# Kernel optimization log

Hardware: AMD Instinct MI355X
Metric: run time of the kernel (lower is better)

The kernel has to match this reference:

```python
import jax, jax.numpy as jnp
import numpy as np

B, N, CQ, H, CH = 1, 256, 128, 4, 32  # batch, n_res, c_q(=c_k=c_v), heads, per-head dim


def setup_inputs() -> dict:
    key = jax.random.key(0)
    ks = jax.random.split(key, 12)
    s = 0.02
    q_x = jax.random.normal(ks[0], (B, N, N, CQ), jnp.float32)
    kv_x = jax.random.normal(ks[1], (B, N, N, CQ), jnp.float32)
    # mask bias: 0 where kept, -1e9 where masked (additive mask)
    keep = jax.random.uniform(ks[2], (B, N, 1, 1, N)) < 0.9
    mask_bias = jnp.where(keep, 0.0, -1e9).astype(jnp.float32)
    triangle_bias = jax.random.normal(ks[3], (B, 1, H, N, N), jnp.float32)
    # projection weights, stored per-head as [H, CH, C_in]
    wq = jax.random.normal(ks[4], (H, CH, CQ), jnp.float32) * s
    wk = jax.random.normal(ks[5], (H, CH, CQ), jnp.float32) * s
    wv = jax.random.normal(ks[6], (H, CH, CQ), jnp.float32) * s
    wg = jax.random.normal(ks[7], (H, CH, CQ), jnp.float32) * s
    bg = jax.random.normal(ks[8], (H, CH), jnp.float32) * s + 1.0  # gating bias init 1
    wo = jax.random.normal(ks[9], (CQ, H * CH), jnp.float32) * s
    bo = jnp.zeros((CQ,), jnp.float32)
    return {"q_x": q_x, "kv_x": kv_x, "mask_bias": mask_bias,
            "triangle_bias": triangle_bias, "wq": wq, "wk": wk, "wv": wv,
            "wg": wg, "bg": bg, "wo": wo, "bo": bo}


def reference(q_x, kv_x, mask_bias, triangle_bias, wq, wk, wv, wg, bg, wo, bo):
    scale = 1.0 / np.sqrt(CH).astype(np.float32)
    # project + split heads: [B,N,Q,C] x [H,D,C] -> [B,N,H,Q,D]
    q = jnp.einsum('bnqc,hdc->bnhqd', q_x, wq) * scale
    k = jnp.einsum('bnkc,hdc->bnhkd', kv_x, wk)
    v = jnp.einsum('bnkc,hdc->bnhkd', kv_x, wv)
    # scores + additive biases (mask_bias broadcasts over h,q; triangle over n)
    a = jnp.einsum('bnhqd,bnhkd->bnhqk', q, k) + mask_bias + triangle_bias
    a = jax.nn.softmax(a, axis=-1)
    o = jnp.einsum('bnhqk,bnhkd->bnhqd', a, v)
    o = jnp.swapaxes(o, -2, -3)  # [B,N,Q,H,D]
    # gating
    g = jax.nn.sigmoid(jnp.einsum('bnqc,hdc->bnqhd', q_x, wg) + bg)
    o = o * g
    o = o.reshape(o.shape[:-2] + (H * CH,))  # [B,N,Q,H*D]
    return jnp.einsum('bnqe,ce->bnqc', o, wo) + bo
```

## Files before the change

### kernel.cpp

```cpp
#include <hip/hip_runtime.h>

#define NRES 256
#define CIN  128
#define NH   4
#define DH   32

#define KST 32
#define VST 264
#define PST 40
#define GST 136

typedef __attribute__((ext_vector_type(4))) float f32x4;
typedef __attribute__((ext_vector_type(8))) short bf16x8;

__device__ __forceinline__ unsigned pkbf(float a, float b) {
    unsigned ua = __builtin_bit_cast(unsigned, a);
    unsigned ub = __builtin_bit_cast(unsigned, b);
    ua += 0x7fffu + ((ua >> 16) & 1u);
    ub += 0x7fffu + ((ub >> 16) & 1u);
    return __builtin_amdgcn_perm(ub, ua, 0x07060302);
}
__device__ __forceinline__ unsigned short f2bfu(float f) {
    unsigned u = __builtin_bit_cast(unsigned, f);
    return (unsigned short)((u + 0x7fffu + ((u >> 16) & 1u)) >> 16);
}
union bfr { unsigned u[4]; bf16x8 v; };
__device__ __forceinline__ bf16x8 ldcvt8(const float* __restrict__ p) {
    f32x4 a = *(const f32x4*)p; f32x4 b = *(const f32x4*)(p + 4);
    bfr r;
    r.u[0] = pkbf(a[0], a[1]); r.u[1] = pkbf(a[2], a[3]);
    r.u[2] = pkbf(b[0], b[1]); r.u[3] = pkbf(b[2], b[3]);
    return r.v;
}
__device__ __forceinline__ bf16x8 ldcvt8s(const float* __restrict__ p, float sc) {
    f32x4 a = *(const f32x4*)p; f32x4 b = *(const f32x4*)(p + 4);
    bfr r;
    r.u[0] = pkbf(a[0] * sc, a[1] * sc); r.u[1] = pkbf(a[2] * sc, a[3] * sc);
    r.u[2] = pkbf(b[0] * sc, b[1] * sc); r.u[3] = pkbf(b[2] * sc, b[3] * sc);
    return r.v;
}
#define MFMA(a, b, c) __builtin_amdgcn_mfma_f32_16x16x32_bf16((a), (b), (c), 0, 0, 0)

__global__ __launch_bounds__(256, 3) void attn_mfma(
    const float* __restrict__ q_x, const float* __restrict__ kv_x,
    const float* __restrict__ mask_bias, const float* __restrict__ tri_bias,
    const float* __restrict__ wq, const float* __restrict__ wk,
    const float* __restrict__ wv, float* __restrict__ o_out)
{
    const int h = blockIdx.x, n = blockIdx.y;
    const int t = threadIdx.x;
    const int lane = t & 63, w = t >> 6;
    const int mrow = lane & 15;
    const int grp  = lane >> 4;
    const int koff = grp * 8;
    const int rbase = grp * 4;
    const int q0 = w * 64;

    __shared__ unsigned short Ks[NRES * KST];
    __shared__ unsigned short Vt[DH * VST];
    __shared__ unsigned short Pt[4 * 32 * PST];
    __shared__ float msk[NRES];

    if (t < 64) *(float4*)&msk[t * 4] = *(const float4*)(mask_bias + n * NRES + t * 4);

    const float* __restrict__ qxn = q_x  + (size_t)n * NRES * CIN;
    const float* __restrict__ kxn = kv_x + (size_t)n * NRES * CIN;
    const float* __restrict__ wqh = wq + h * DH * CIN;
    const float* __restrict__ wkh = wk + h * DH * CIN;
    const float* __restrict__ wvh = wv + h * DH * CIN;

    f32x4 aq_[4][2], ak_[4][2], av_[4][2];
    const f32x4 zf = {0.f, 0.f, 0.f, 0.f};
    #pragma unroll
    for (int qt = 0; qt < 4; ++qt)
        #pragma unroll
        for (int dt = 0; dt < 2; ++dt) { aq_[qt][dt] = zf; ak_[qt][dt] = zf; av_[qt][dt] = zf; }

    const float qsc = 0.17677669529663687f;
    #pragma unroll
    for (int ct = 0; ct < 4; ++ct) {
        const int c0 = ct * 32 + koff;
        bf16x8 bq0 = ldcvt8s(wqh + mrow * CIN + c0, qsc);
        bf16x8 bq1 = ldcvt8s(wqh + (16 + mrow) * CIN + c0, qsc);
        bf16x8 bk0 = ldcvt8(wkh + mrow * CIN + c0);
        bf16x8 bk1 = ldcvt8(wkh + (16 + mrow) * CIN + c0);
        bf16x8 bv0 = ldcvt8(wvh + mrow * CIN + c0);
        bf16x8 bv1 = ldcvt8(wvh + (16 + mrow) * CIN + c0);
        #pragma unroll
        for (int qt = 0; qt < 4; ++qt) {
            bf16x8 aX = ldcvt8(qxn + (q0 + qt * 16 + mrow) * CIN + c0);
            aq_[qt][0] = MFMA(aX, bq0, aq_[qt][0]);
            aq_[qt][1] = MFMA(aX, bq1, aq_[qt][1]);
            bf16x8 aK = ldcvt8(kxn + (q0 + qt * 16 + mrow) * CIN + c0);
            ak_[qt][0] = MFMA(aK, bk0, ak_[qt][0]);
            ak_[qt][1] = MFMA(aK, bk1, ak_[qt][1]);
            av_[qt][0] = MFMA(aK, bv0, av_[qt][0]);
            av_[qt][1] = MFMA(aK, bv1, av_[qt][1]);
        }
    }

    #pragma unroll
    for (int qt = 0; qt < 4; ++qt)
        #pragma unroll
        for (int dt = 0; dt < 2; ++dt)
            #pragma unroll
            for (int r = 0; r < 4; ++r) {
                const int row = q0 + qt * 16 + rbase + r;
                const int d = dt * 16 + mrow;
                Ks[row * KST + d] = f2bfu(ak_[qt][dt][r]);
                Vt[d * VST + row] = f2bfu(av_[qt][dt][r]);
            }

    unsigned short* __restrict__ pw = &Pt[w * 32 * PST];
    bf16x8 aq[4];
    #pragma unroll
    for (int h2 = 0; h2 < 2; ++h2) {
        #pragma unroll
        for (int j = 0; j < 2; ++j) {
            const int qt = h2 * 2 + j;
            #pragma unroll
            for (int dt = 0; dt < 2; ++dt)
                #pragma unroll
                for (int r = 0; r < 4; ++r)
                    pw[(j * 16 + rbase + r) * PST + dt * 16 + mrow] = f2bfu(aq_[qt][dt][r]);
        }
        asm volatile("s_waitcnt lgkmcnt(0)" ::: "memory");
        #pragma unroll
        for (int j = 0; j < 2; ++j)
            aq[h2 * 2 + j] = *(const bf16x8*)&pw[(j * 16 + mrow) * PST + koff];
        asm volatile("s_waitcnt lgkmcnt(0)" ::: "memory");
    }
    __syncthreads();

    f32x4 oa[4][2], ls4[4];
    #pragma unroll
    for (int qt = 0; qt < 4; ++qt) { oa[qt][0] = zf; oa[qt][1] = zf; ls4[qt] = zf; }

    const float* __restrict__ trih = tri_bias + (size_t)h * NRES * NRES;

    for (int kt = 0; kt < 8; ++kt) {
        const int kb = kt * 32;
        bf16x8 bk0 = *(const bf16x8*)&Ks[(kb + mrow) * KST + koff];
        bf16x8 bk1 = *(const bf16x8*)&Ks[(kb + 16 + mrow) * KST + koff];
        bf16x8 bv0 = *(const bf16x8*)&Vt[mrow * VST + kb + koff];
        bf16x8 bv1 = *(const bf16x8*)&Vt[(16 + mrow) * VST + kb + koff];
        const float mb0 = msk[kb + mrow] - 8.f;
        const float mb1 = msk[kb + 16 + mrow] - 8.f;

        #pragma unroll
        for (int h2 = 0; h2 < 2; ++h2) {
            float tr0[2][4], tr1[2][4];
            #pragma unroll
            for (int j = 0; j < 2; ++j) {
                const int qt = h2 * 2 + j;
                const float* __restrict__ trow =
                    trih + (q0 + qt * 16 + rbase) * NRES + kb + mrow;
                #pragma unroll
                for (int r = 0; r < 4; ++r) {
                    tr0[j][r] = trow[r * NRES];
                    tr1[j][r] = trow[r * NRES + 16];
                }
            }
            #pragma unroll
            for (int j = 0; j < 2; ++j) {
                const int qt = h2 * 2 + j;
                f32x4 s0 = MFMA(aq[qt], bk0, zf);
                f32x4 s1 = MFMA(aq[qt], bk1, zf);
                #pragma unroll
                for (int r = 0; r < 4; ++r) {
                    s0[r] = __expf(s0[r] + tr0[j][r] + mb0);
                    s1[r] = __expf(s1[r] + tr1[j][r] + mb1);
                }
                ls4[qt] += s0 + s1;
                #pragma unroll
                for (int r = 0; r < 4; ++r) {
                    pw[(j * 16 + rbase + r) * PST + mrow]      = f2bfu(s0[r]);
                    pw[(j * 16 + rbase + r) * PST + 16 + mrow] = f2bfu(s1[r]);
                }
            }
            asm volatile("s_waitcnt lgkmcnt(0)" ::: "memory");
            #pragma unroll
            for (int j = 0; j < 2; ++j) {
                const int qt = h2 * 2 + j;
                bf16x8 pa = *(const bf16x8*)&pw[(j * 16 + mrow) * PST + koff];
                oa[qt][0] = MFMA(pa, bv0, oa[qt][0]);
                oa[qt][1] = MFMA(pa, bv1, oa[qt][1]);
            }
        }
    }

    float* __restrict__ orow = o_out + (size_t)n * NRES * CIN + h * DH;
    #pragma unroll
    for (int qt = 0; qt < 4; ++qt) {
        f32x4 lv = ls4[qt];
        #pragma unroll
        for (int xm = 1; xm < 16; xm <<= 1) {
            lv[0] += __shfl_xor(lv[0], xm, 64);
            lv[1] += __shfl_xor(lv[1], xm, 64);
            lv[2] += __shfl_xor(lv[2], xm, 64);
            lv[3] += __shfl_xor(lv[3], xm, 64);
        }
        #pragma unroll
        for (int r = 0; r < 4; ++r) {
            const float inv = 1.f / lv[r];
            const int q = q0 + qt * 16 + rbase + r;
            orow[q * CIN + mrow]      = oa[qt][0][r] * inv;
            orow[q * CIN + 16 + mrow] = oa[qt][1][r] * inv;
        }
    }
}

__global__ __launch_bounds__(256, 4) void gate_out(
    const float* __restrict__ q_x, const float* __restrict__ wg,
    const float* __restrict__ bg, const float* __restrict__ wo,
    const float* __restrict__ bo, float* __restrict__ io)
{
    const int t = threadIdx.x;
    const int lane = t & 63, w = t >> 6;
    const int mrow = lane & 15, grp = lane >> 4;
    const int koff = grp * 8, rbase = grp * 4;
    const int r0 = blockIdx.x * 128 + w * 32;

    __shared__ unsigned short Gt[4 * 32 * GST];
    unsigned short* __restrict__ gw = &Gt[w * 32 * GST];

    const f32x4 zf = {0.f, 0.f, 0.f, 0.f};
    f32x4 acc[2][8];
    #pragma unroll
    for (int at = 0; at < 2; ++at)
        #pragma unroll
        for (int nt = 0; nt < 8; ++nt) acc[at][nt] = zf;

    #pragma unroll
    for (int ks = 0; ks < 4; ++ks) {
        const int c0 = ks * 32 + koff;
        bf16x8 ax0 = ldcvt8(q_x + (size_t)(r0 + mrow) * CIN + c0);
        bf16x8 ax1 = ldcvt8(q_x + (size_t)(r0 + 16 + mrow) * CIN + c0);
        #pragma unroll
        for (int nt = 0; nt < 8; ++nt) {
            bf16x8 bw = ldcvt8(wg + (nt * 16 + mrow) * CIN + c0);
            acc[0][nt] = MFMA(ax0, bw, acc[0][nt]);
            acc[1][nt] = MFMA(ax1, bw, acc[1][nt]);
        }
    }

    #pragma unroll
    for (int nt = 0; nt < 8; ++nt) {
        const float bge = bg[nt * 16 + mrow];
        #pragma unroll
        for (int at = 0; at < 2; ++at)
            #pragma unroll
            for (int r = 0; r < 4; ++r) {
                const int qg = r0 + at * 16 + rbase + r;
                const float ov = io[(size_t)qg * CIN + nt * 16 + mrow];
                const float g = 1.f / (1.f + __expf(-(acc[at][nt][r] + bge)));
                gw[(at * 16 + rbase + r) * GST + nt * 16 + mrow] = f2bfu(ov * g);
            }
    }
    asm volatile("s_waitcnt lgkmcnt(0)" ::: "memory");

    f32x4 acc2[2][8];
    #pragma unroll
    for (int at = 0; at < 2; ++at)
        #pragma unroll
        for (int nt = 0; nt < 8; ++nt) acc2[at][nt] = zf;

    #pragma unroll
    for (int ks = 0; ks < 4; ++ks) {
        const int e0 = ks * 32 + koff;
        bf16x8 ag0 = *(const bf16x8*)&gw[mrow * GST + e0];
        bf16x8 ag1 = *(const bf16x8*)&gw[(16 + mrow) * GST + e0];
        #pragma unroll
        for (int nt = 0; nt < 8; ++nt) {
            bf16x8 bw = ldcvt8(wo + (nt * 16 + mrow) * CIN + e0);
            acc2[0][nt] = MFMA(ag0, bw, acc2[0][nt]);
            acc2[1][nt] = MFMA(ag1, bw, acc2[1][nt]);
        }
    }

    #pragma unroll
    for (int nt = 0; nt < 8; ++nt) {
        const float boc = bo[nt * 16 + mrow];
        #pragma unroll
        for (int at = 0; at < 2; ++at)
            #pragma unroll
            for (int r = 0; r < 4; ++r)
                io[(size_t)(r0 + at * 16 + rbase + r) * CIN + nt * 16 + mrow] =
                    acc2[at][nt][r] + boc;
    }
}

extern "C" void kernel_launch(void* const* d_in, const int* in_sizes, int n_in,
                              void* d_out, int out_size, void* d_ws, size_t ws_size,
                              hipStream_t stream) {
    const float* q_x  = (const float*)d_in[0];
    const float* kv_x = (const float*)d_in[1];
    const float* mask = (const float*)d_in[2];
    const float* tri  = (const float*)d_in[3];
    const float* wq   = (const float*)d_in[4];
    const float* wk   = (const float*)d_in[5];
    const float* wv   = (const float*)d_in[6];
    const float* wg   = (const float*)d_in[7];
    const float* bg   = (const float*)d_in[8];
    const float* wo   = (const float*)d_in[9];
    const float* bo   = (const float*)d_in[10];
    float* out = (float*)d_out;

    attn_mfma<<<dim3(NH, NRES), 256, 0, stream>>>(q_x, kv_x, mask, tri, wq, wk, wv, out);
    gate_out<<<(NRES * NRES) / 128, 256, 0, stream>>>(q_x, wg, bg, wo, bo, out);
}
```

Before: 270.6 us.

## Hoist QKV and gate projections out of per-head attention into workspace kernels

Restructures the pipeline into four kernels. A one-time bf16 conversion of the weights is followed by a batched projection kernel that computes Q, K, V and the sigmoid gate once per row and writes them to workspace as bf16. A flash-style attention kernel then reads them, applies the gate in its epilogue, and a final kernel does the output projection. Previously each head's block recomputed the K/V projections over the full kv row, and the gate GEMM was done separately. The trade is extra global traffic for the bf16 intermediates, a large workspace requirement, and a fallback to the old path when the workspace is too small.

```diff
diff --git a/kernel.cpp b/kernel.cpp
--- a/kernel.cpp
+++ b/kernel.cpp
@@ -5,13 +5,18 @@
 #define NH   4
 #define DH   32
 
-#define KST 32
-#define VST 264
-#define PST 40
-#define GST 136
-
 typedef __attribute__((ext_vector_type(4))) float f32x4;
 typedef __attribute__((ext_vector_type(8))) short bf16x8;
+typedef unsigned short u16;
+
+#define U_WQG 0
+#define U_WKV 32768
+#define U_WWO 65536
+#define U_QB  131072
+#define U_KB  (U_QB + 8388608)
+#define U_VT  (U_KB + 8388608)
+#define U_GB  (U_VT + 8388608)
+#define WS_NEED ((size_t)(U_GB + 8388608) * 2)
 
 __device__ __forceinline__ unsigned pkbf(float a, float b) {
     unsigned ua = __builtin_bit_cast(unsigned, a);
@@ -20,9 +25,13 @@
     ub += 0x7fffu + ((ub >> 16) & 1u);
     return __builtin_amdgcn_perm(ub, ua, 0x07060302);
 }
-__device__ __forceinline__ unsigned short f2bfu(float f) {
+__device__ __forceinline__ u16 f2bfu(float f) {
     unsigned u = __builtin_bit_cast(unsigned, f);
-    return (unsigned short)((u + 0x7fffu + ((u >> 16) & 1u)) >> 16);
+    return (u16)((u + 0x7fffu + ((u >> 16) & 1u)) >> 16);
+}
+__device__ __forceinline__ float bf2f(u16 v) {
+    unsigned u = ((unsigned)v) << 16;
+    return __builtin_bit_cast(float, u);
 }
 union bfr { unsigned u[4]; bf16x8 v; };
 __device__ __forceinline__ bf16x8 ldcvt8(const float* __restrict__ p) {
@@ -41,7 +50,249 @@
 }
 #define MFMA(a, b, c) __builtin_amdgcn_mfma_f32_16x16x32_bf16((a), (b), (c), 0, 0, 0)
 
-__global__ __launch_bounds__(256, 3) void attn_mfma(
+__global__ void wconv(const float* __restrict__ wq, const float* __restrict__ wk,
+                      const float* __restrict__ wv, const float* __restrict__ wg,
+                      const float* __restrict__ wo, u16* __restrict__ ws)
+{
+    const int i0 = (blockIdx.x * 256 + threadIdx.x) * 8;
+    const float qsc = 0.17677669529663687f;
+    const float* src; u16* dst; float sc = 1.f;
+    if (i0 < 32768) {
+        const int e = i0 >> 7, c = i0 & 127;
+        src = (e < 128 ? wq + e * CIN : wg + (e - 128) * CIN) + c;
+        if (e < 128) sc = qsc;
+        dst = ws + U_WQG + i0;
+    } else if (i0 < 65536) {
+        const int j = i0 - 32768, e = j >> 7, c = j & 127;
+        src = (e < 128 ? wk + e * CIN : wv + (e - 128) * CIN) + c;
+        dst = ws + U_WKV + j;
+    } else {
+        const int j = i0 - 65536;
+        src = wo + j; dst = ws + U_WWO + j;
+    }
+    *(bf16x8*)dst = ldcvt8s(src, sc);
+}
+
+__global__ __launch_bounds__(256, 4) void proj(
+    const float* __restrict__ q_x, const float* __restrict__ kv_x,
+    const float* __restrict__ bg, u16* __restrict__ ws)
+{
+    const int t = threadIdx.x, lane = t & 63, w = t >> 6;
+    const int mrow = lane & 15, grp = lane >> 4;
+    const int koff = grp * 8, rbase = grp * 4;
+    const int R0 = blockIdx.x * 64 + w * 16;
+    const int ysel = blockIdx.y;
+    const float* __restrict__ src = ysel ? kv_x : q_x;
+    const u16* __restrict__ W = ws + (ysel ? U_WKV : U_WQG);
+
+    const f32x4 zf = {0.f, 0.f, 0.f, 0.f};
+    f32x4 acc[16];
+    #pragma unroll
+    for (int nt = 0; nt < 16; ++nt) acc[nt] = zf;
+
+    #pragma unroll
+    for (int ct = 0; ct < 4; ++ct) {
+        const int c0 = ct * 32 + koff;
+        bf16x8 aX = ldcvt8(src + (size_t)(R0 + mrow) * CIN + c0);
+        #pragma unroll
+        for (int nt = 0; nt < 16; ++nt) {
+            bf16x8 bw = *(const bf16x8*)(W + (nt * 16 + mrow) * CIN + c0);
+            acc[nt] = MFMA(aX, bw, acc[nt]);
+        }
+    }
+
+    if (!ysel) {
+        #pragma unroll
+        for (int nt = 0; nt < 8; ++nt) {
+            const int e = nt * 16 + mrow;
+            #pragma unroll
+            for (int r = 0; r < 4; ++r)
+                ws[U_QB + (size_t)(R0 + rbase + r) * CIN + e] = f2bfu(acc[nt][r]);
+        }
+        #pragma unroll
+        for (int nt = 8; nt < 16; ++nt) {
+            const int e = (nt - 8) * 16 + mrow;
+            const float b = bg[e];
+            #pragma unroll
+            for (int r = 0; r < 4; ++r) {
+                const float g = 1.f / (1.f + __expf(-(acc[nt][r] + b)));
+                ws[U_GB + (size_t)(R0 + rbase + r) * CIN + e] = f2bfu(g);
+            }
+        }
+    } else {
+        #pragma unroll
+        for (int nt = 0; nt < 8; ++nt) {
+            const int e = nt * 16 + mrow;
+            #pragma unroll
+            for (int r = 0; r < 4; ++r)
+                ws[U_KB + (size_t)(R0 + rbase + r) * CIN + e] = f2bfu(acc[nt][r]);
+        }
+        const int n = R0 >> 8, k0 = (R0 & 255) + rbase;
+        #pragma unroll
+        for (int nt = 8; nt < 16; ++nt) {
+            const int dcol = (nt - 8) * 16 + mrow;
+            uint2 v;
+            v.x = pkbf(acc[nt][0], acc[nt][1]);
+            v.y = pkbf(acc[nt][2], acc[nt][3]);
+            *(uint2*)&ws[U_VT + ((size_t)n * 128 + dcol) * 256 + k0] = v;
+        }
+    }
+}
+
+#define PST 40
+__global__ __launch_bounds__(256, 4) void flash(
+    const u16* __restrict__ ws, const float* __restrict__ mask_bias,
+    const float* __restrict__ tri_bias, float* __restrict__ o_out)
+{
+    const int h = blockIdx.x, n = blockIdx.y;
+    const int t = threadIdx.x, lane = t & 63, w = t >> 6;
+    const int mrow = lane & 15, grp = lane >> 4;
+    const int koff = grp * 8, rbase = grp * 4;
+    const int q0 = w * 64;
+
+    __shared__ u16 Pt[4 * 64 * PST];
+    __shared__ float msk[NRES];
+
+    if (t < 64) *(float4*)&msk[t * 4] = *(const float4*)(mask_bias + n * NRES + t * 4);
+
+    const u16* __restrict__ Qb = ws + U_QB + (size_t)n * NRES * CIN;
+    const u16* __restrict__ Kb = ws + U_KB + (size_t)n * NRES * CIN;
+    const u16* __restrict__ Vt = ws + U_VT + (size_t)n * 128 * 256;
+    const u16* __restrict__ Gb = ws + U_GB + (size_t)n * NRES * CIN;
+    const float* __restrict__ trih = tri_bias + (size_t)h * NRES * NRES;
+
+    bf16x8 aq[4];
+    #pragma unroll
+    for (int qt = 0; qt < 4; ++qt)
+        aq[qt] = *(const bf16x8*)(Qb + (size_t)(q0 + qt * 16 + mrow) * CIN + h * DH + koff);
+    __syncthreads();
+
+    const f32x4 zf = {0.f, 0.f, 0.f, 0.f};
+    f32x4 oa[4][2], ls4[4];
+    #pragma unroll
+    for (int qt = 0; qt < 4; ++qt) { oa[qt][0] = zf; oa[qt][1] = zf; ls4[qt] = zf; }
+
+    u16* __restrict__ pw = &Pt[w * 64 * PST];
+
+    for (int kt = 0; kt < 8; ++kt) {
+        const int kb = kt * 32;
+        bf16x8 bk0 = *(const bf16x8*)(Kb + (size_t)(kb + mrow) * CIN + h * DH + koff);
+        bf16x8 bk1 = *(const bf16x8*)(Kb + (size_t)(kb + 16 + mrow) * CIN + h * DH + koff);
+        bf16x8 bv0 = *(const bf16x8*)(Vt + (size_t)(h * DH + mrow) * NRES + kb + koff);
+        bf16x8 bv1 = *(const bf16x8*)(Vt + (size_t)(h * DH + 16 + mrow) * NRES + kb + koff);
+        const float mb0 = msk[kb + mrow] - 8.f;
+        const float mb1 = msk[kb + 16 + mrow] - 8.f;
+
+        #pragma unroll
+        for (int h2 = 0; h2 < 2; ++h2) {
+            float tr0[2][4], tr1[2][4];
+            #pragma unroll
+            for (int j = 0; j < 2; ++j) {
+                const int qt = h2 * 2 + j;
+                const float* __restrict__ trow =
+                    trih + (q0 + qt * 16 + rbase) * NRES + kb + mrow;
+                #pragma unroll
+                for (int r = 0; r < 4; ++r) {
+                    tr0[j][r] = trow[r * NRES];
+                    tr1[j][r] = trow[r * NRES + 16];
+                }
+            }
+            #pragma unroll
+            for (int j = 0; j < 2; ++j) {
+                const int qt = h2 * 2 + j;
+                f32x4 s0 = MFMA(aq[qt], bk0, zf);
+                f32x4 s1 = MFMA(aq[qt], bk1, zf);
+                #pragma unroll
+                for (int r = 0; r < 4; ++r) {
+                    s0[r] = __expf(s0[r] + tr0[j][r] + mb0);
+                    s1[r] = __expf(s1[r] + tr1[j][r] + mb1);
+                }
+                ls4[qt] += s0 + s1;
+                #pragma unroll
+                for (int r = 0; r < 4; ++r) {
+                    pw[(qt * 16 + rbase + r) * PST + mrow]      = f2bfu(s0[r]);
+                    pw[(qt * 16 + rbase + r) * PST + 16 + mrow] = f2bfu(s1[r]);
+                }
+            }
+        }
+        asm volatile("s_waitcnt lgkmcnt(0)" ::: "memory");
+        #pragma unroll
+        for (int qt = 0; qt < 4; ++qt) {
+            bf16x8 pa = *(const bf16x8*)&pw[(qt * 16 + mrow) * PST + koff];
+            oa[qt][0] = MFMA(pa, bv0, oa[qt][0]);
+            oa[qt][1] = MFMA(pa, bv1, oa[qt][1]);
+        }
+    }
+
+    float* __restrict__ orow = o_out + (size_t)n * NRES * CIN + h * DH;
+    #pragma unroll
+    for (int qt = 0; qt < 4; ++qt) {
+        f32x4 lv = ls4[qt];
+        #pragma unroll
+        for (int xm = 1; xm < 16; xm <<= 1) {
+            lv[0] += __shfl_xor(lv[0], xm, 64);
+            lv[1] += __shfl_xor(lv[1], xm, 64);
+            lv[2] += __shfl_xor(lv[2], xm, 64);
+            lv[3] += __shfl_xor(lv[3], xm, 64);
+        }
+        #pragma unroll
+        for (int r = 0; r < 4; ++r) {
+            const float inv = 1.f / lv[r];
+            const int q = q0 + qt * 16 + rbase + r;
+            const float g0 = bf2f(Gb[(size_t)q * CIN + h * DH + mrow]);
+            const float g1 = bf2f(Gb[(size_t)q * CIN + h * DH + 16 + mrow]);
+            orow[q * CIN + mrow]      = oa[qt][0][r] * inv * g0;
+            orow[q * CIN + 16 + mrow] = oa[qt][1][r] * inv * g1;
+        }
+    }
+}
+
+__global__ __launch_bounds__(256, 4) void gout(
+    const u16* __restrict__ ws, const float* __restrict__ bo, float* io)
+{
+    const int t = threadIdx.x, lane = t & 63, w = t >> 6;
+    const int mrow = lane & 15, grp = lane >> 4;
+    const int koff = grp * 8, rbase = grp * 4;
+    const int r0 = blockIdx.x * 128 + w * 32;
+    const u16* __restrict__ Wo = ws + U_WWO;
+
+    const f32x4 zf = {0.f, 0.f, 0.f, 0.f};
+    f32x4 acc[2][8];
+    #pragma unroll
+    for (int at = 0; at < 2; ++at)
+        #pragma unroll
+        for (int nt = 0; nt < 8; ++nt) acc[at][nt] = zf;
+
+    #pragma unroll
+    for (int ks = 0; ks < 4; ++ks) {
+        const int e0 = ks * 32 + koff;
+        bf16x8 a0 = ldcvt8(io + (size_t)(r0 + mrow) * CIN + e0);
+        bf16x8 a1 = ldcvt8(io + (size_t)(r0 + 16 + mrow) * CIN + e0);
+        #pragma unroll
+        for (int nt = 0; nt < 8; ++nt) {
+            bf16x8 bw = *(const bf16x8*)(Wo + (nt * 16 + mrow) * CIN + e0);
+            acc[0][nt] = MFMA(a0, bw, acc[0][nt]);
+            acc[1][nt] = MFMA(a1, bw, acc[1][nt]);
+        }
+    }
+
+    #pragma unroll
+    for (int nt = 0; nt < 8; ++nt) {
+        const float bc = bo[nt * 16 + mrow];
+        #pragma unroll
+        for (int at = 0; at < 2; ++at)
+            #pragma unroll
+            for (int r = 0; r < 4; ++r)
+                io[(size_t)(r0 + at * 16 + rbase + r) * CIN + nt * 16 + mrow] =
+                    acc[at][nt][r] + bc;
+    }
+}
+
+#define KST 32
+#define VST 264
+#define GST 136
+
+__global__ __launch_bounds__(256, 3) void attn_fb(
     const float* __restrict__ q_x, const float* __restrict__ kv_x,
     const float* __restrict__ mask_bias, const float* __restrict__ tri_bias,
     const float* __restrict__ wq, const float* __restrict__ wk,
@@ -56,9 +307,9 @@
     const int rbase = grp * 4;
     const int q0 = w * 64;
 
-    __shared__ unsigned short Ks[NRES * KST];
-    __shared__ unsigned short Vt[DH * VST];
-    __shared__ unsigned short Pt[4 * 32 * PST];
+    __shared__ u16 Ks[NRES * KST];
+    __shared__ u16 Vt[DH * VST];
+    __shared__ u16 Ptb[4 * 32 * PST];
     __shared__ float msk[NRES];
 
     if (t < 64) *(float4*)&msk[t * 4] = *(const float4*)(mask_bias + n * NRES + t * 4);
@@ -111,7 +362,7 @@
                 Vt[d * VST + row] = f2bfu(av_[qt][dt][r]);
             }
 
-    unsigned short* __restrict__ pw = &Pt[w * 32 * PST];
+    u16* __restrict__ pw = &Ptb[w * 32 * PST];
     bf16x8 aq[4];
     #pragma unroll
     for (int h2 = 0; h2 < 2; ++h2) {
@@ -210,10 +461,10 @@
     }
 }
 
-__global__ __launch_bounds__(256, 4) void gate_out(
+__global__ __launch_bounds__(256, 4) void gate_fb(
     const float* __restrict__ q_x, const float* __restrict__ wg,
     const float* __restrict__ bg, const float* __restrict__ wo,
-    const float* __restrict__ bo, float* __restrict__ io)
+    const float* __restrict__ bo, float* io)
 {
     const int t = threadIdx.x;
     const int lane = t & 63, w = t >> 6;
@@ -221,8 +472,8 @@
     const int koff = grp * 8, rbase = grp * 4;
     const int r0 = blockIdx.x * 128 + w * 32;
 
-    __shared__ unsigned short Gt[4 * 32 * GST];
-    unsigned short* __restrict__ gw = &Gt[w * 32 * GST];
+    __shared__ u16 Gt[4 * 32 * GST];
+    u16* __restrict__ gw = &Gt[w * 32 * GST];
 
     const f32x4 zf = {0.f, 0.f, 0.f, 0.f};
     f32x4 acc[2][8];
@@ -306,6 +557,14 @@
     const float* bo   = (const float*)d_in[10];
     float* out = (float*)d_out;
 
-    attn_mfma<<<dim3(NH, NRES), 256, 0, stream>>>(q_x, kv_x, mask, tri, wq, wk, wv, out);
-    gate_out<<<(NRES * NRES) / 128, 256, 0, stream>>>(q_x, wg, bg, wo, bo, out);
-}
+    if (ws_size >= WS_NEED) {
+        u16* ws16 = (u16*)d_ws;
+        wconv<<<40, 256, 0, stream>>>(wq, wk, wv, wg, wo, ws16);
+        proj<<<dim3(1024, 2), 256, 0, stream>>>(q_x, kv_x, bg, ws16);
+        flash<<<dim3(NH, NRES), 256, 0, stream>>>(ws16, mask, tri, out);
+        gout<<<512, 256, 0, stream>>>(ws16, bo, out);
+    } else {
+        attn_fb<<<dim3(NH, NRES), 256, 0, stream>>>(q_x, kv_x, mask, tri, wq, wk, wv, out);
+        gate_fb<<<(NRES * NRES) / 128, 256, 0, stream>>>(q_x, wg, bg, wo, bo, out);
+    }
+}
```

Measured after the change: 246.2 us. 9.0% less time.
